# Optimization experiments

Measured on AMD Instinct MI355X. Metric: run time of the kernel, lower is better.

Reference implementation:

```python
import jax, jax.numpy as jnp
import numpy as np

N_BINS = 15
N = 1_000_000
C = 128


def setup_inputs() -> dict:
    key = jax.random.key(0)
    k1, k2 = jax.random.split(key)
    logits = jax.random.normal(k1, (N, C), dtype=jnp.float32)
    labels = jax.random.randint(k2, (N,), 0, C, dtype=jnp.int64)
    return {"logits": logits, "labels": labels}


def reference(logits, labels):
    # softmax -> per-sample confidence (max prob) and prediction (argmax)
    probs = jax.nn.softmax(logits, axis=1)
    confidences = jnp.max(probs, axis=1)          # [N]
    predictions = jnp.argmax(probs, axis=1)       # [N]
    accuracies = (predictions == labels).astype(jnp.float32)  # [N]

    # bin_lowers = linspace(0,1,n_bins+1)[:-1]; sample falls in bin i if
    # conf >= lower_i and conf < lower_{i+1} (last bin closed at 1.0).
    bin_lowers = jnp.linspace(0.0, 1.0, N_BINS + 1)[:-1]
    bin_idx = jnp.searchsorted(bin_lowers, confidences, side="right") - 1
    bin_idx = jnp.clip(bin_idx, 0, N_BINS - 1)

    correct = jax.ops.segment_sum(accuracies, bin_idx, num_segments=N_BINS)
    total = jax.ops.segment_sum(jnp.ones_like(accuracies), bin_idx, num_segments=N_BINS)
    # column 0: correct count in bin; column 1: incorrect count in bin
    bin_stats = jnp.stack([correct, total - correct], axis=1)  # [N_BINS, 2]
    return bin_stats
```

## Files before the change

kernel.cpp:

```cpp
#include <hip/hip_runtime.h>

#define N_BINS 15
#define NCLASS 128

__global__ void zero_out_kernel(float* __restrict__ out) {
    int i = threadIdx.x;
    if (i < 2 * N_BINS) out[i] = 0.0f;
}

__global__ __launch_bounds__(256) void conf_hist_kernel(
        const float* __restrict__ logits,
        const int* __restrict__ labels,
        float* __restrict__ out,
        int n) {
    __shared__ int hist[2 * N_BINS];
    if (threadIdx.x < 2 * N_BINS) hist[threadIdx.x] = 0;
    __syncthreads();

    const int lane = threadIdx.x & 63;
    const int waveInBlock = threadIdx.x >> 6;
    const int wavesPerBlock = blockDim.x >> 6;
    const int wave = blockIdx.x * wavesPerBlock + waveInBlock;
    const int numWaves = gridDim.x * wavesPerBlock;

    for (int s = wave; s < n; s += numWaves) {
        const float2 v = *(const float2*)(logits + (size_t)s * NCLASS + lane * 2);

        float m; int mi;
        if (v.x >= v.y) { m = v.x; mi = lane * 2; }
        else            { m = v.y; mi = lane * 2 + 1; }
        #pragma unroll
        for (int off = 32; off > 0; off >>= 1) {
            float om = __shfl_xor(m, off);
            int   oi = __shfl_xor(mi, off);
            if (om > m || (om == m && oi < mi)) { m = om; mi = oi; }
        }

        float e = __expf(v.x - m) + __expf(v.y - m);
        #pragma unroll
        for (int off = 32; off > 0; off >>= 1) e += __shfl_xor(e, off);

        if (lane == 0) {
            float conf = 1.0f / e;
            int bin = (int)(conf * (float)N_BINS);
            bin = bin > (N_BINS - 1) ? (N_BINS - 1) : (bin < 0 ? 0 : bin);
            int col = (mi == labels[s]) ? 0 : 1;
            atomicAdd(&hist[bin * 2 + col], 1);
        }
    }

    __syncthreads();
    if (threadIdx.x < 2 * N_BINS) {
        int c = hist[threadIdx.x];
        if (c != 0) atomicAdd(&out[threadIdx.x], (float)c);
    }
}

extern "C" void kernel_launch(void* const* d_in, const int* in_sizes, int n_in,
                              void* d_out, int out_size, void* d_ws, size_t ws_size,
                              hipStream_t stream) {
    const float* logits = (const float*)d_in[0];
    const int*   labels = (const int*)d_in[1];
    float* out = (float*)d_out;
    const int n = in_sizes[1];

    zero_out_kernel<<<1, 64, 0, stream>>>(out);

    const int block = 256;
    const int grid = 2048;
    conf_hist_kernel<<<grid, block, 0, stream>>>(logits, labels, out, n);
}
```

Before: 752.9 us.

## Process eight samples per wave with 16-lane groups and float4 loads

Each wave now handles eight samples per iteration, with four 16-lane groups each reducing one row using two float4 loads per lane instead of one float2 per lane across the whole wave. This cuts the shuffle reduction depth from six to four steps and keeps more independent memory loads in flight per wave. In exchange, each lane holds more registers and does a serial 8-element max and exp. Four lanes per wave now issue shared atomics where one did before.

```diff
diff --git a/kernel.cpp b/kernel.cpp
--- a/kernel.cpp
+++ b/kernel.cpp
@@ -6,6 +6,42 @@
 __global__ void zero_out_kernel(float* __restrict__ out) {
     int i = threadIdx.x;
     if (i < 2 * N_BINS) out[i] = 0.0f;
+}
+
+__device__ __forceinline__ void reduce_sample(float4 a, float4 b, int t,
+                                              float& conf, int& argmax) {
+    float m = a.x; int mi = 0;
+    if (a.y > m) { m = a.y; mi = 1; }
+    if (a.z > m) { m = a.z; mi = 2; }
+    if (a.w > m) { m = a.w; mi = 3; }
+    if (b.x > m) { m = b.x; mi = 4; }
+    if (b.y > m) { m = b.y; mi = 5; }
+    if (b.z > m) { m = b.z; mi = 6; }
+    if (b.w > m) { m = b.w; mi = 7; }
+    mi += t * 8;
+
+    #pragma unroll
+    for (int off = 1; off < 16; off <<= 1) {
+        float om = __shfl_xor(m, off);
+        int   oi = __shfl_xor(mi, off);
+        if (om > m || (om == m && oi < mi)) { m = om; mi = oi; }
+    }
+
+    float e = __expf(a.x - m) + __expf(a.y - m) + __expf(a.z - m) + __expf(a.w - m)
+            + __expf(b.x - m) + __expf(b.y - m) + __expf(b.z - m) + __expf(b.w - m);
+    #pragma unroll
+    for (int off = 1; off < 16; off <<= 1) e += __shfl_xor(e, off);
+
+    conf = 1.0f / e;
+    argmax = mi;
+}
+
+__device__ __forceinline__ void bin_sample(float conf, int argmax, int label,
+                                           int* hist) {
+    int bin = (int)(conf * (float)N_BINS);
+    bin = bin > (N_BINS - 1) ? (N_BINS - 1) : (bin < 0 ? 0 : bin);
+    int col = (argmax == label) ? 0 : 1;
+    atomicAdd(&hist[bin * 2 + col], 1);
 }
 
 __global__ __launch_bounds__(256) void conf_hist_kernel(
@@ -18,34 +54,37 @@
     __syncthreads();
 
     const int lane = threadIdx.x & 63;
-    const int waveInBlock = threadIdx.x >> 6;
+    const int g = lane >> 4;
+    const int t = lane & 15;
     const int wavesPerBlock = blockDim.x >> 6;
-    const int wave = blockIdx.x * wavesPerBlock + waveInBlock;
+    const int wave = blockIdx.x * wavesPerBlock + (threadIdx.x >> 6);
     const int numWaves = gridDim.x * wavesPerBlock;
 
-    for (int s = wave; s < n; s += numWaves) {
-        const float2 v = *(const float2*)(logits + (size_t)s * NCLASS + lane * 2);
+    for (int base = wave * 8; base < n; base += numWaves * 8) {
+        const int s0 = base + g;
+        const int s1 = base + 4 + g;
+        const bool v0 = s0 < n;
+        const bool v1 = s1 < n;
 
-        float m; int mi;
-        if (v.x >= v.y) { m = v.x; mi = lane * 2; }
-        else            { m = v.y; mi = lane * 2 + 1; }
-        #pragma unroll
-        for (int off = 32; off > 0; off >>= 1) {
-            float om = __shfl_xor(m, off);
-            int   oi = __shfl_xor(mi, off);
-            if (om > m || (om == m && oi < mi)) { m = om; mi = oi; }
+        float4 a0, b0, a1, b1;
+        if (v0) {
+            const float4* p = (const float4*)(logits + (size_t)s0 * NCLASS + t * 8);
+            a0 = p[0]; b0 = p[1];
+        }
+        if (v1) {
+            const float4* p = (const float4*)(logits + (size_t)s1 * NCLASS + t * 8);
+            a1 = p[0]; b1 = p[1];
         }
 
-        float e = __expf(v.x - m) + __expf(v.y - m);
-        #pragma unroll
-        for (int off = 32; off > 0; off >>= 1) e += __shfl_xor(e, off);
-
-        if (lane == 0) {
-            float conf = 1.0f / e;
-            int bin = (int)(conf * (float)N_BINS);
-            bin = bin > (N_BINS - 1) ? (N_BINS - 1) : (bin < 0 ? 0 : bin);
-            int col = (mi == labels[s]) ? 0 : 1;
-            atomicAdd(&hist[bin * 2 + col], 1);
+        if (v0) {
+            float conf; int mi;
+            reduce_sample(a0, b0, t, conf, mi);
+            if (t == 0) bin_sample(conf, mi, labels[s0], hist);
+        }
+        if (v1) {
+            float conf; int mi;
+            reduce_sample(a1, b1, t, conf, mi);
+            if (t == 0) bin_sample(conf, mi, labels[s1], hist);
         }
     }
 
```

Result: faster. 654.1 us (-13.1%).

## Process 16 rows per wave with 4-lane quads and DPP reductions

Applied to the files above, without the earlier changes.

Each wave now handles 16 rows at once, giving each row to a 4-lane quad. Every lane loads 8 float4s and does most of the max/argmax and exp-sum work in registers. Cross-lane reduction shrinks from 6-step wave-wide shuffles to two DPP quad-permute steps. This cuts per-row shuffle and instruction overhead and adds memory-level parallelism per wave, at the cost of more registers and a different intra-row tie-break order for argmax.

```diff
diff --git a/kernel.cpp b/kernel.cpp
--- a/kernel.cpp
+++ b/kernel.cpp
@@ -6,6 +6,19 @@
 __global__ void zero_out_kernel(float* __restrict__ out) {
     int i = threadIdx.x;
     if (i < 2 * N_BINS) out[i] = 0.0f;
+}
+
+__device__ __forceinline__ int dpp_xor1_i(int x) {
+    return __builtin_amdgcn_mov_dpp(x, 0xB1, 0xF, 0xF, true);
+}
+__device__ __forceinline__ int dpp_xor2_i(int x) {
+    return __builtin_amdgcn_mov_dpp(x, 0x4E, 0xF, 0xF, true);
+}
+__device__ __forceinline__ float dpp_xor1_f(float x) {
+    return __int_as_float(dpp_xor1_i(__float_as_int(x)));
+}
+__device__ __forceinline__ float dpp_xor2_f(float x) {
+    return __int_as_float(dpp_xor2_i(__float_as_int(x)));
 }
 
 __global__ __launch_bounds__(256) void conf_hist_kernel(
@@ -18,34 +31,65 @@
     __syncthreads();
 
     const int lane = threadIdx.x & 63;
-    const int waveInBlock = threadIdx.x >> 6;
+    const int quad = lane >> 2;
+    const int t = lane & 3;
     const int wavesPerBlock = blockDim.x >> 6;
-    const int wave = blockIdx.x * wavesPerBlock + waveInBlock;
+    const int wave = blockIdx.x * wavesPerBlock + (threadIdx.x >> 6);
     const int numWaves = gridDim.x * wavesPerBlock;
 
-    for (int s = wave; s < n; s += numWaves) {
-        const float2 v = *(const float2*)(logits + (size_t)s * NCLASS + lane * 2);
+    for (int base = wave * 16; base < n; base += numWaves * 16) {
+        const int s = base + quad;
+        if (s < n) {
+            const float* row = logits + (size_t)s * NCLASS + t * 4;
+            float4 c[8];
+            #pragma unroll
+            for (int j = 0; j < 8; ++j)
+                c[j] = *(const float4*)(row + j * 16);
 
-        float m; int mi;
-        if (v.x >= v.y) { m = v.x; mi = lane * 2; }
-        else            { m = v.y; mi = lane * 2 + 1; }
-        #pragma unroll
-        for (int off = 32; off > 0; off >>= 1) {
-            float om = __shfl_xor(m, off);
-            int   oi = __shfl_xor(mi, off);
-            if (om > m || (om == m && oi < mi)) { m = om; mi = oi; }
-        }
+            float m[8]; int mi[8];
+            #pragma unroll
+            for (int j = 0; j < 8; ++j) {
+                float mm = c[j].x; int ii = 0;
+                if (c[j].y > mm) { mm = c[j].y; ii = 1; }
+                if (c[j].z > mm) { mm = c[j].z; ii = 2; }
+                if (c[j].w > mm) { mm = c[j].w; ii = 3; }
+                m[j] = mm; mi[j] = j * 16 + t * 4 + ii;
+            }
+            #pragma unroll
+            for (int stp = 1; stp < 8; stp <<= 1) {
+                #pragma unroll
+                for (int j = 0; j < 8; j += 2 * stp) {
+                    if (m[j + stp] > m[j]) { m[j] = m[j + stp]; mi[j] = mi[j + stp]; }
+                }
+            }
+            float bm = m[0]; int bi = mi[0];
 
-        float e = __expf(v.x - m) + __expf(v.y - m);
-        #pragma unroll
-        for (int off = 32; off > 0; off >>= 1) e += __shfl_xor(e, off);
+            {
+                float om = dpp_xor1_f(bm); int oi = dpp_xor1_i(bi);
+                if (om > bm || (om == bm && oi < bi)) { bm = om; bi = oi; }
+            }
+            {
+                float om = dpp_xor2_f(bm); int oi = dpp_xor2_i(bi);
+                if (om > bm || (om == bm && oi < bi)) { bm = om; bi = oi; }
+            }
 
-        if (lane == 0) {
-            float conf = 1.0f / e;
-            int bin = (int)(conf * (float)N_BINS);
-            bin = bin > (N_BINS - 1) ? (N_BINS - 1) : (bin < 0 ? 0 : bin);
-            int col = (mi == labels[s]) ? 0 : 1;
-            atomicAdd(&hist[bin * 2 + col], 1);
+            float s4[8];
+            #pragma unroll
+            for (int j = 0; j < 8; ++j)
+                s4[j] = (__expf(c[j].x - bm) + __expf(c[j].y - bm))
+                      + (__expf(c[j].z - bm) + __expf(c[j].w - bm));
+            float e = ((s4[0] + s4[1]) + (s4[2] + s4[3]))
+                    + ((s4[4] + s4[5]) + (s4[6] + s4[7]));
+            e += dpp_xor1_f(e);
+            e += dpp_xor2_f(e);
+
+            if (t == 0) {
+                float conf = 1.0f / e;
+                int bin = (int)(conf * (float)N_BINS);
+                bin = bin > (N_BINS - 1) ? (N_BINS - 1) : (bin < 0 ? 0 : bin);
+                int col = (bi == labels[s]) ? 0 : 1;
+                atomicAdd(&hist[bin * 2 + col], 1);
+            }
         }
     }
 
```

Result: faster. 647.0 us (-14.1%).
